# Kernel tuning notes

Hardware: AMD Instinct MI355X
Metric: run time of the kernel (lower is better)

Reference implementation:

```python
import jax, jax.numpy as jnp
import numpy as np

B, T, C, E = 8, 8192, 256, 64
CAPACITY_FACTOR = 1.25
TOP_K = 2


def setup_inputs() -> dict:
    key = jax.random.key(0)
    k1, k2, k3 = jax.random.split(key, 3)
    x = jax.random.normal(k1, (B, T, C), dtype=jnp.float32)
    W_gate = jax.random.normal(k2, (C, E), dtype=jnp.float32) / np.sqrt(C)
    W_experts = jax.random.normal(k3, (E, C, C), dtype=jnp.float32) / np.sqrt(C)
    return {"x": x, "W_gate": W_gate, "W_experts": W_experts}


def reference(x, W_gate, W_experts):
    b, t, c = x.shape
    e = W_gate.shape[1]
    n = b * t              # tokens
    s = n * TOP_K          # assignment slots, ordered (token i, slot j) like the torch loop
    capacity = max(1, int(CAPACITY_FACTOR * s / e))  # static python int

    logits = x @ W_gate                              # [B,T,E]
    gates = jax.nn.softmax(logits, axis=-1)
    scores, indices = jax.lax.top_k(gates, TOP_K)    # [B,T,2] (values are raw gate probs, no renorm)

    x_flat = x.reshape(n, c)
    eid = indices.reshape(s)                         # expert id per assignment, FIFO order i*2+j
    sc = scores.reshape(s)
    tok = jnp.repeat(jnp.arange(n), TOP_K)           # source token per assignment

    # FIFO rank of each assignment within its expert (matches the python capacity loop)
    onehot = jax.nn.one_hot(eid, e, dtype=jnp.int32)          # [S,E]
    rank = jnp.cumsum(onehot, axis=0)[jnp.arange(s), eid] - 1  # prior count of same expert
    keep = rank < capacity                                     # capacity-dropped tokens

    # Scatter tokens into per-expert buffers [E*capacity, C]; dropped slots go OOB -> 'drop'
    buf_idx = jnp.where(keep, eid * capacity + rank, e * capacity)
    buf = jnp.zeros((e * capacity, c), x.dtype).at[buf_idx].set(x_flat[tok], mode="drop")

    # Grouped GEMM: one Linear(C,C) per expert
    y = jnp.einsum("eck,ekd->ecd", buf.reshape(e, capacity, c), W_experts)
    y = y.reshape(e * capacity, c)

    # Gather back, scale by gate score, scatter-add into token positions
    safe_idx = jnp.where(keep, buf_idx, 0)
    contrib = jnp.where(keep[:, None], y[safe_idx] * sc[:, None], jnp.zeros((), x.dtype))
    combined = jnp.zeros((n, c), x.dtype).at[tok].add(contrib).reshape(b, t, c)

    load = gates.mean(axis=(0, 1))                  # [E]
    aux_loss = jnp.mean((load - 1.0 / e) ** 2)      # mse vs uniform
    return combined, aux_loss
```

## Files before the change

### kernel.cpp

```cpp
#include <hip/hip_runtime.h>
#include <stdint.h>

#define N_TOK   65536
#define S_SLOTS 131072
#define NEXP    64
#define CDIM    256
#define CAP     2560
#define NCHUNK  1024

typedef unsigned short u16;
typedef float    fvec4  __attribute__((ext_vector_type(4)));
typedef float    f32x4  __attribute__((ext_vector_type(4)));
typedef __bf16   bf16x8 __attribute__((ext_vector_type(8)));
typedef unsigned short u16x4 __attribute__((ext_vector_type(4)));

typedef __attribute__((address_space(1))) const void gvoid_t;
typedef __attribute__((address_space(3))) void       svoid_t;

__device__ __forceinline__ u16 f2bf(float f) {
  uint32_t u = __builtin_bit_cast(uint32_t, f);
  u += 0x7fffu + ((u >> 16) & 1u);
  return (u16)(u >> 16);
}
__device__ __forceinline__ float bf2f(u16 h) {
  return __builtin_bit_cast(float, (uint32_t)h << 16);
}
__device__ __forceinline__ void gload16(const void* g, void* l) {
  __builtin_amdgcn_global_load_lds(
      reinterpret_cast<gvoid_t*>(reinterpret_cast<uintptr_t>(g)),
      reinterpret_cast<svoid_t*>(reinterpret_cast<uintptr_t>(l)),
      16, 0, 0);
}

__global__ __launch_bounds__(256) void gating_kernel(
    const float* __restrict__ x, const float* __restrict__ Wg,
    u16* __restrict__ x_bf16, float* __restrict__ slot_score,
    int* __restrict__ slot_eid, float* __restrict__ load_g,
    int* __restrict__ chunk_hist)
{
  __shared__ float smem[8448];
  __shared__ int   hist_s[64];
  float* W_s   = smem;
  float* A_s   = smem + 4096;
  float* L_s   = smem;
  float* PMAXs = smem + 4160;
  float* PV1   = smem + 4416;
  int*   PI1   = (int*)(smem + 4672);
  float* PV2   = smem + 4928;
  int*   PI2   = (int*)(smem + 5184);
  float* PSUM  = smem + 5440;
  float* RINVs = smem + 5696;
  float* PLOAD = smem + 5760;

  const int t  = threadIdx.x;
  const int m0 = blockIdx.x * 64;
  const int ty = t >> 4, tx = t & 15;

  if (t < 64) hist_s[t] = 0;

  float acc[4][4];
#pragma unroll
  for (int j = 0; j < 4; ++j)
#pragma unroll
    for (int i = 0; i < 4; ++i) acc[j][i] = 0.f;

  for (int kt = 0; kt < 4; ++kt) {
    const int k0 = kt * 64;
#pragma unroll
    for (int p = 0; p < 4; ++p) {
      int idx = p * 1024 + t * 4;
      int kk = idx >> 6, e = idx & 63;
      *(fvec4*)&W_s[kk * 64 + e] = *(const fvec4*)&Wg[(size_t)(k0 + kk) * 64 + e];
    }
#pragma unroll
    for (int p = 0; p < 4; ++p) {
      int idx = p * 1024 + t * 4;
      int m = idx >> 6, k = idx & 63;
      fvec4 v = *(const fvec4*)&x[(size_t)(m0 + m) * 256 + k0 + k];
      *(fvec4*)&A_s[m * 68 + k] = v;
      u16x4 h;
      h.x = f2bf(v.x); h.y = f2bf(v.y); h.z = f2bf(v.z); h.w = f2bf(v.w);
      *(u16x4*)&x_bf16[(size_t)(m0 + m) * 256 + k0 + k] = h;
    }
    __syncthreads();
#pragma unroll
    for (int k4 = 0; k4 < 16; ++k4) {
      fvec4 av[4], bv[4];
#pragma unroll
      for (int j = 0; j < 4; ++j)
        av[j] = *(const fvec4*)&A_s[(ty * 4 + j) * 68 + k4 * 4];
#pragma unroll
      for (int kk = 0; kk < 4; ++kk)
        bv[kk] = *(const fvec4*)&W_s[(k4 * 4 + kk) * 64 + tx * 4];
#pragma unroll
      for (int j = 0; j < 4; ++j)
#pragma unroll
        for (int i = 0; i < 4; ++i) {
          acc[j][i] = fmaf(av[j][0], bv[0][i], acc[j][i]);
          acc[j][i] = fmaf(av[j][1], bv[1][i], acc[j][i]);
          acc[j][i] = fmaf(av[j][2], bv[2][i], acc[j][i]);
          acc[j][i] = fmaf(av[j][3], bv[3][i], acc[j][i]);
        }
    }
    __syncthreads();
  }

#pragma unroll
  for (int j = 0; j < 4; ++j)
#pragma unroll
    for (int i = 0; i < 4; ++i)
      L_s[(ty * 4 + j) * 65 + tx * 4 + i] = acc[j][i];
  __syncthreads();

  const int w = t >> 6, lane = t & 63;

  float pm = -3.4e38f, a1 = -3.4e38f, a2 = -3.4e38f;
  int   j1 = 0, j2 = 0;
#pragma unroll
  for (int ii = 0; ii < 16; ++ii) {
    int e = w * 16 + ii;
    float lg = L_s[lane * 65 + e];
    pm = fmaxf(pm, lg);
    if (lg > a1)      { a2 = a1; j2 = j1; a1 = lg; j1 = e; }
    else if (lg > a2) { a2 = lg; j2 = e; }
  }
  PMAXs[w * 64 + lane] = pm;
  PV1[w * 64 + lane] = a1; PI1[w * 64 + lane] = j1;
  PV2[w * 64 + lane] = a2; PI2[w * 64 + lane] = j2;
  __syncthreads();

  float m  = PMAXs[lane];
  float v1 = PV1[lane]; int i1 = PI1[lane];
  float v2 = PV2[lane]; int i2 = PI2[lane];
#pragma unroll
  for (int ww = 1; ww < 4; ++ww) {
    m = fmaxf(m, PMAXs[ww * 64 + lane]);
    float b1 = PV1[ww * 64 + lane]; int bi1 = PI1[ww * 64 + lane];
    float b2 = PV2[ww * 64 + lane]; int bi2 = PI2[ww * 64 + lane];
    if (b1 > v1) {
      if (v1 >= b2) { v2 = v1; i2 = i1; } else { v2 = b2; i2 = bi2; }
      v1 = b1; i1 = bi1;
    } else if (b1 > v2) { v2 = b1; i2 = bi1; }
  }

  float s = 0.f;
#pragma unroll
  for (int ii = 0; ii < 16; ++ii) {
    int e = w * 16 + ii;
    float E = __expf(L_s[lane * 65 + e] - m);
    L_s[lane * 65 + e] = E;
    s += E;
  }
  PSUM[w * 64 + lane] = s;
  __syncthreads();

  if (w == 0) {
    float rs = PSUM[lane] + PSUM[64 + lane] + PSUM[128 + lane] + PSUM[192 + lane];
    float ri = 1.0f / rs;
    RINVs[lane] = ri;
    float sc1 = L_s[lane * 65 + i1] * ri;
    float sc2 = L_s[lane * 65 + i2] * ri;
    int tg = m0 + lane;
    slot_eid[2 * tg]     = i1;
    slot_eid[2 * tg + 1] = i2;
    slot_score[2 * tg]     = sc1;
    slot_score[2 * tg + 1] = sc2;
    atomicAdd(&hist_s[i1], 1);
    atomicAdd(&hist_s[i2], 1);
  }
  __syncthreads();

  {
    float sl = 0.f;
#pragma unroll
    for (int jj = 0; jj < 16; ++jj) {
      int j = w * 16 + jj;
      sl = fmaf(L_s[j * 65 + lane], RINVs[j], sl);
    }
    PLOAD[t] = sl;
  }
  __syncthreads();
  if (t < 64) {
    float sl = PLOAD[t] + PLOAD[64 + t] + PLOAD[128 + t] + PLOAD[192 + t];
    atomicAdd(&load_g[t], sl);
    chunk_hist[blockIdx.x * 64 + t] = hist_s[t];
  }
}

__global__ __launch_bounds__(256) void wtrans_kernel(
    const float* __restrict__ W, u16* __restrict__ WT)
{
  __shared__ float tile[64 * 65];
  const int b = blockIdx.x;
  const int e = b >> 4, tt = b & 15;
  const int k0 = (tt >> 2) * 64, d0 = (tt & 3) * 64;
  const int t = threadIdx.x;
  const int j = t & 63, i0 = t >> 6;
  const float* We = W + (size_t)e * 65536;
#pragma unroll
  for (int p = 0; p < 16; ++p) {
    int i = p * 4 + i0;
    tile[i * 65 + j] = We[(size_t)(k0 + i) * 256 + d0 + j];
  }
  __syncthreads();
  u16* WTe = WT + (size_t)e * 65536;
#pragma unroll
  for (int p = 0; p < 16; ++p) {
    int d = p * 4 + i0;
    WTe[(size_t)(d0 + d) * 256 + k0 + j] = f2bf(tile[j * 65 + d]);
  }
}

__global__ __launch_bounds__(256) void scan_kernel(int* __restrict__ hist)
{
  const int e = blockIdx.x;
  const int t = threadIdx.x;
  const int lane = t & 63, w = t >> 6;
  int h[4];
#pragma unroll
  for (int i = 0; i < 4; ++i) h[i] = hist[(t * 4 + i) * 64 + e];
  int local = h[0] + h[1] + h[2] + h[3];
  int v = local;
#pragma unroll
  for (int off = 1; off < 64; off <<= 1) {
    int u = __shfl_up(v, off);
    if (lane >= off) v += u;
  }
  __shared__ int wtot[4];
  if (lane == 63) wtot[w] = v;
  __syncthreads();
  int woff = 0;
  for (int i = 0; i < w; ++i) woff += wtot[i];
  int excl = woff + v - local;
  hist[(t * 4 + 0) * 64 + e] = excl;
  hist[(t * 4 + 1) * 64 + e] = excl + h[0];
  hist[(t * 4 + 2) * 64 + e] = excl + h[0] + h[1];
  hist[(t * 4 + 3) * 64 + e] = excl + h[0] + h[1] + h[2];
}

__global__ __launch_bounds__(128) void rank_kernel(
    const int* __restrict__ slot_eid, const int* __restrict__ base,
    int* __restrict__ slot2buf, int* __restrict__ row_token)
{
  const int c = blockIdx.x;
  const int t = threadIdx.x;
  const int s = c * 128 + t;
  const int lane = t & 63, w = t >> 6;
  const int e = slot_eid[s];
  __shared__ int hist0[64];
  if (t < 64) hist0[t] = 0;
  __syncthreads();
  int rank = 0, cnt = 0;
#pragma unroll
  for (int k = 0; k < 64; ++k) {
    int eo = __shfl(e, k);
    bool m = (eo == e);
    rank += (m && k < lane) ? 1 : 0;
    cnt  += m ? 1 : 0;
  }
  if (w == 0 && rank == cnt - 1) hist0[e] = cnt;
  __syncthreads();
  int g = base[c * 64 + e] + rank + (w ? hist0[e] : 0);
  if (g < CAP) {
    slot2buf[s] = e * CAP + g;
    row_token[e * CAP + g] = s >> 1;
  } else {
    slot2buf[s] = -1;
  }
}

__global__ __launch_bounds__(256) void gemm_kernel(
    const u16* __restrict__ x_bf16, const u16* __restrict__ WT,
    const int* __restrict__ row_token, u16* __restrict__ y)
{
  __shared__ u16 A_s[128 * 32];
  __shared__ u16 B_s[128 * 32];
  __shared__ int tok_s[128];

  const int b = blockIdx.x;
  const int e = b / 40;
  const int r = b % 40;
  const int m0 = (r >> 1) * 128, n0 = (r & 1) * 128;
  const int t = threadIdx.x;

  if (t < 128) tok_s[t] = row_token[e * CAP + m0 + t];
  __syncthreads();

  const int w = t >> 6, lane = t & 63;
  const int rsub = lane >> 2;
  const int koff = (lane & 3) * 8;

  const int ra0 = w * 32 + rsub;
  const int ra1 = ra0 + 16;
  const char* pa0 = (const char*)(x_bf16 + (size_t)tok_s[ra0] * 256 + koff);
  const char* pa1 = (const char*)(x_bf16 + (size_t)tok_s[ra1] * 256 + koff);
  const u16* WTe = WT + (size_t)e * 65536;
  const char* pb0 = (const char*)(WTe + (size_t)(n0 + ra0) * 256 + koff);
  const char* pb1 = (const char*)(WTe + (size_t)(n0 + ra1) * 256 + koff);

  char* ldsA0 = (char*)A_s + (w * 32) * 64;
  char* ldsA1 = (char*)A_s + (w * 32 + 16) * 64;
  char* ldsB0 = (char*)B_s + (w * 32) * 64;
  char* ldsB1 = (char*)B_s + (w * 32 + 16) * 64;

  const int wm = w & 1, wn = w >> 1;
  const int lr = lane & 15, q = lane >> 4;

  f32x4 acc[4][4];
#pragma unroll
  for (int mt = 0; mt < 4; ++mt)
#pragma unroll
    for (int nt = 0; nt < 4; ++nt) acc[mt][nt] = (f32x4){0.f, 0.f, 0.f, 0.f};

  for (int kt = 0; kt < 8; ++kt) {
    gload16(pa0, ldsA0);
    gload16(pa1, ldsA1);
    gload16(pb0, ldsB0);
    gload16(pb1, ldsB1);
    __syncthreads();
    bf16x8 af[4], bg[4];
#pragma unroll
    for (int mt = 0; mt < 4; ++mt)
      af[mt] = *(const bf16x8*)&A_s[(wm * 64 + mt * 16 + lr) * 32 + q * 8];
#pragma unroll
    for (int nt = 0; nt < 4; ++nt)
      bg[nt] = *(const bf16x8*)&B_s[(wn * 64 + nt * 16 + lr) * 32 + q * 8];
#pragma unroll
    for (int mt = 0; mt < 4; ++mt)
#pragma unroll
      for (int nt = 0; nt < 4; ++nt)
        acc[mt][nt] = __builtin_amdgcn_mfma_f32_16x16x32_bf16(
            af[mt], bg[nt], acc[mt][nt], 0, 0, 0);
    __syncthreads();
    pa0 += 64; pa1 += 64; pb0 += 64; pb1 += 64;
  }

  u16* ye = y + (size_t)e * CAP * 256;
#pragma unroll
  for (int mt = 0; mt < 4; ++mt) {
    int grow = m0 + wm * 64 + mt * 16 + q * 4;
#pragma unroll
    for (int nt = 0; nt < 4; ++nt) {
      int gcol = n0 + wn * 64 + nt * 16 + lr;
#pragma unroll
      for (int rr = 0; rr < 4; ++rr)
        ye[(size_t)(grow + rr) * 256 + gcol] = f2bf(acc[mt][nt][rr]);
    }
  }
}

__global__ __launch_bounds__(256) void combine_kernel(
    const u16* __restrict__ y, const int* __restrict__ slot2buf,
    const float* __restrict__ slot_score, float* __restrict__ out)
{
  const int tok  = blockIdx.x * 4 + (threadIdx.x >> 6);
  const int lane = threadIdx.x & 63;
  const int   p0 = slot2buf[2 * tok],   p1 = slot2buf[2 * tok + 1];
  const float s0 = slot_score[2 * tok], s1 = slot_score[2 * tok + 1];
  float o0 = 0.f, o1 = 0.f, o2 = 0.f, o3 = 0.f;
  if (p0 >= 0) {
    u16x4 h = *(const u16x4*)&y[(size_t)p0 * 256 + lane * 4];
    o0 = fmaf(s0, bf2f(h.x), o0); o1 = fmaf(s0, bf2f(h.y), o1);
    o2 = fmaf(s0, bf2f(h.z), o2); o3 = fmaf(s0, bf2f(h.w), o3);
  }
  if (p1 >= 0) {
    u16x4 h = *(const u16x4*)&y[(size_t)p1 * 256 + lane * 4];
    o0 = fmaf(s1, bf2f(h.x), o0); o1 = fmaf(s1, bf2f(h.y), o1);
    o2 = fmaf(s1, bf2f(h.z), o2); o3 = fmaf(s1, bf2f(h.w), o3);
  }
  fvec4 o = {o0, o1, o2, o3};
  *(fvec4*)&out[(size_t)tok * 256 + lane * 4] = o;
}

__global__ __launch_bounds__(64) void aux_kernel(
    const float* __restrict__ load_g, float* __restrict__ out_aux)
{
  const int lane = threadIdx.x;
  float l = load_g[lane] * (1.0f / 65536.0f) - (1.0f / 64.0f);
  float v = l * l;
#pragma unroll
  for (int off = 1; off < 64; off <<= 1) v += __shfl_xor(v, off);
  if (lane == 0) out_aux[0] = v * (1.0f / 64.0f);
}

extern "C" void kernel_launch(void* const* d_in, const int* in_sizes, int n_in,
                              void* d_out, int out_size, void* d_ws, size_t ws_size,
                              hipStream_t stream)
{
  const float* x  = (const float*)d_in[0];
  const float* Wg = (const float*)d_in[1];
  const float* We = (const float*)d_in[2];
  float* out = (float*)d_out;

  char* ws = (char*)d_ws;
  float* slot_score = (float*)(ws + 0);
  int*   slot_eid   = (int*)(ws + 524288);
  int*   slot2buf   = (int*)(ws + 1048576);
  int*   row_token  = (int*)(ws + 1572864);
  float* load_g     = (float*)(ws + 2228224);
  int*   chunk_hist = (int*)(ws + 2359296);
  u16*   x_bf16     = (u16*)(ws + 4194304);
  u16*   WT         = (u16*)(ws + 37748736);
  u16*   y          = (u16*)(ws + 46137344);

  hipMemsetAsync(row_token, 0, 655360, stream);
  hipMemsetAsync(load_g, 0, 256, stream);

  gating_kernel<<<1024, 256, 0, stream>>>(x, Wg, x_bf16, slot_score, slot_eid,
                                          load_g, chunk_hist);
  wtrans_kernel<<<1024, 256, 0, stream>>>(We, WT);
  scan_kernel<<<64, 256, 0, stream>>>(chunk_hist);
  rank_kernel<<<1024, 128, 0, stream>>>(slot_eid, chunk_hist, slot2buf, row_token);
  gemm_kernel<<<2560, 256, 0, stream>>>(x_bf16, WT, row_token, y);
  combine_kernel<<<16384, 256, 0, stream>>>(y, slot2buf, slot_score, out);
  aux_kernel<<<1, 64, 0, stream>>>(load_g, out + 16777216);
}
```

Baseline: 239.0 us.

## Compute gating logits with split-bf16 MFMA instead of fp32 FMA

Replaces the fp32 scalar-FMA gating GEMM with bf16 MFMA instructions. Each fp32 operand is split into three bf16 parts (hi/mid/lo) and six cross products are accumulated to keep near-fp32 accuracy. A new small kernel pre-splits and transposes W_gate, and x tiles are loaded into LDS with direct global-to-LDS loads. The aim is to cut the compute cost of the gating matmul, at the price of an extra launch, the on-the-fly splitting work, and a small risk of top-k ties resolving differently.

Measured after the change: 242.2 us. Within noise of the previous version (+1.3%).

```diff
diff --git a/kernel.cpp b/kernel.cpp
--- a/kernel.cpp
+++ b/kernel.cpp
@@ -13,6 +13,7 @@
 typedef float    f32x4  __attribute__((ext_vector_type(4)));
 typedef __bf16   bf16x8 __attribute__((ext_vector_type(8)));
 typedef unsigned short u16x4 __attribute__((ext_vector_type(4)));
+typedef unsigned short u16x8 __attribute__((ext_vector_type(8)));
 
 typedef __attribute__((address_space(1))) const void gvoid_t;
 typedef __attribute__((address_space(3))) void       svoid_t;
@@ -32,87 +33,128 @@
       16, 0, 0);
 }
 
+__global__ __launch_bounds__(256) void wgsplit_kernel(
+    const float* __restrict__ Wg, u16* __restrict__ WgT_h,
+    u16* __restrict__ WgT_m, u16* __restrict__ WgT_l)
+{
+  __shared__ float tile[64 * 65];
+  const int k0 = blockIdx.x * 64;
+  const int t = threadIdx.x;
+  const int j = t & 63, i0 = t >> 6;
+#pragma unroll
+  for (int p = 0; p < 16; ++p) {
+    int i = p * 4 + i0;
+    tile[i * 65 + j] = Wg[(size_t)(k0 + i) * 64 + j];
+  }
+  __syncthreads();
+  const int e = t >> 2, kb = (t & 3) * 16;
+#pragma unroll
+  for (int p = 0; p < 16; ++p) {
+    int kk = kb + p;
+    float v = tile[kk * 65 + e];
+    u16 h  = f2bf(v); float r1 = v  - bf2f(h);
+    u16 md = f2bf(r1); float r2 = r1 - bf2f(md);
+    u16 l  = f2bf(r2);
+    size_t off = (size_t)e * 256 + k0 + kk;
+    WgT_h[off] = h; WgT_m[off] = md; WgT_l[off] = l;
+  }
+}
+
 __global__ __launch_bounds__(256) void gating_kernel(
-    const float* __restrict__ x, const float* __restrict__ Wg,
+    const float* __restrict__ x,
+    const u16* __restrict__ WgT_h, const u16* __restrict__ WgT_m,
+    const u16* __restrict__ WgT_l,
     u16* __restrict__ x_bf16, float* __restrict__ slot_score,
     int* __restrict__ slot_eid, float* __restrict__ load_g,
     int* __restrict__ chunk_hist)
 {
-  __shared__ float smem[8448];
-  __shared__ int   hist_s[64];
-  float* W_s   = smem;
-  float* A_s   = smem + 4096;
-  float* L_s   = smem;
-  float* PMAXs = smem + 4160;
-  float* PV1   = smem + 4416;
-  int*   PI1   = (int*)(smem + 4672);
-  float* PV2   = smem + 4928;
-  int*   PI2   = (int*)(smem + 5184);
-  float* PSUM  = smem + 5440;
-  float* RINVs = smem + 5696;
-  float* PLOAD = smem + 5760;
+  __shared__ char smem[32768];
+  __shared__ int  hist_s[64];
+  float* X_s = (float*)smem;
+  u16* A_h = (u16*)(smem + 8192);
+  u16* A_m = (u16*)(smem + 12288);
+  u16* A_l = (u16*)(smem + 16384);
+  u16* B_h = (u16*)(smem + 20480);
+  u16* B_m = (u16*)(smem + 24576);
+  u16* B_l = (u16*)(smem + 28672);
+  float* tf   = (float*)smem;
+  float* L_s  = tf;
+  float* PMAX = tf + 4160;
+  float* PV1  = tf + 4416;
+  int*   PI1  = (int*)(tf + 4672);
+  float* PV2  = tf + 4928;
+  int*   PI2  = (int*)(tf + 5184);
+  float* PSUM = tf + 5440;
+  float* RINV = tf + 5696;
+  float* PLOAD= tf + 5760;
 
   const int t  = threadIdx.x;
   const int m0 = blockIdx.x * 64;
-  const int ty = t >> 4, tx = t & 15;
+  const int w = t >> 6, lane = t & 63;
+  const int lr = lane & 15, q = lane >> 4;
+  const int srow = t >> 2;
+  const int scol = (t & 3) * 8;
 
   if (t < 64) hist_s[t] = 0;
 
-  float acc[4][4];
-#pragma unroll
-  for (int j = 0; j < 4; ++j)
-#pragma unroll
-    for (int i = 0; i < 4; ++i) acc[j][i] = 0.f;
-
-  for (int kt = 0; kt < 4; ++kt) {
-    const int k0 = kt * 64;
-#pragma unroll
-    for (int p = 0; p < 4; ++p) {
-      int idx = p * 1024 + t * 4;
-      int kk = idx >> 6, e = idx & 63;
-      *(fvec4*)&W_s[kk * 64 + e] = *(const fvec4*)&Wg[(size_t)(k0 + kk) * 64 + e];
+  f32x4 acc[4];
+#pragma unroll
+  for (int nt = 0; nt < 4; ++nt) acc[nt] = (f32x4){0.f, 0.f, 0.f, 0.f};
+
+  const float* gx = x + (size_t)(m0 + w * 16 + (lane >> 3)) * 256 + (lane & 7) * 4;
+  const size_t wgoff = (size_t)(w * 16 + (lane >> 2)) * 256 + (lane & 3) * 8;
+
+  for (int kt = 0; kt < 8; ++kt) {
+    __syncthreads();
+    gload16(gx + kt * 32,            (char*)X_s + w * 2048);
+    gload16(gx + kt * 32 + 8 * 256,  (char*)X_s + w * 2048 + 1024);
+    gload16(WgT_h + wgoff + kt * 32, (char*)B_h + w * 1024);
+    gload16(WgT_m + wgoff + kt * 32, (char*)B_m + w * 1024);
+    gload16(WgT_l + wgoff + kt * 32, (char*)B_l + w * 1024);
+    __syncthreads();
+
+    {
+      float v[8];
+      *(fvec4*)&v[0] = *(const fvec4*)&X_s[srow * 32 + scol];
+      *(fvec4*)&v[4] = *(const fvec4*)&X_s[srow * 32 + scol + 4];
+      u16x8 hv, mv, lv;
+#pragma unroll
+      for (int i = 0; i < 8; ++i) {
+        float f = v[i];
+        u16 h  = f2bf(f); float r1 = f  - bf2f(h);
+        u16 md = f2bf(r1); float r2 = r1 - bf2f(md);
+        hv[i] = h; mv[i] = md; lv[i] = f2bf(r2);
+      }
+      *(u16x8*)&A_h[srow * 32 + scol] = hv;
+      *(u16x8*)&A_m[srow * 32 + scol] = mv;
+      *(u16x8*)&A_l[srow * 32 + scol] = lv;
+      *(u16x8*)&x_bf16[(size_t)(m0 + srow) * 256 + kt * 32 + scol] = hv;
     }
-#pragma unroll
-    for (int p = 0; p < 4; ++p) {
-      int idx = p * 1024 + t * 4;
-      int m = idx >> 6, k = idx & 63;
-      fvec4 v = *(const fvec4*)&x[(size_t)(m0 + m) * 256 + k0 + k];
-      *(fvec4*)&A_s[m * 68 + k] = v;
-      u16x4 h;
-      h.x = f2bf(v.x); h.y = f2bf(v.y); h.z = f2bf(v.z); h.w = f2bf(v.w);
-      *(u16x4*)&x_bf16[(size_t)(m0 + m) * 256 + k0 + k] = h;
+
+    bf16x8 ah = *(const bf16x8*)&A_h[(w * 16 + lr) * 32 + q * 8];
+    bf16x8 am = *(const bf16x8*)&A_m[(w * 16 + lr) * 32 + q * 8];
+    bf16x8 al = *(const bf16x8*)&A_l[(w * 16 + lr) * 32 + q * 8];
+#pragma unroll
+    for (int nt = 0; nt < 4; ++nt) {
+      bf16x8 bh = *(const bf16x8*)&B_h[(nt * 16 + lr) * 32 + q * 8];
+      bf16x8 bm = *(const bf16x8*)&B_m[(nt * 16 + lr) * 32 + q * 8];
+      bf16x8 bl = *(const bf16x8*)&B_l[(nt * 16 + lr) * 32 + q * 8];
+      acc[nt] = __builtin_amdgcn_mfma_f32_16x16x32_bf16(ah, bh, acc[nt], 0, 0, 0);
+      acc[nt] = __builtin_amdgcn_mfma_f32_16x16x32_bf16(ah, bm, acc[nt], 0, 0, 0);
+      acc[nt] = __builtin_amdgcn_mfma_f32_16x16x32_bf16(am, bh, acc[nt], 0, 0, 0);
+      acc[nt] = __builtin_amdgcn_mfma_f32_16x16x32_bf16(am, bm, acc[nt], 0, 0, 0);
+      acc[nt] = __builtin_amdgcn_mfma_f32_16x16x32_bf16(ah, bl, acc[nt], 0, 0, 0);
+      acc[nt] = __builtin_amdgcn_mfma_f32_16x16x32_bf16(al, bh, acc[nt], 0, 0, 0);
     }
-    __syncthreads();
-#pragma unroll
-    for (int k4 = 0; k4 < 16; ++k4) {
-      fvec4 av[4], bv[4];
-#pragma unroll
-      for (int j = 0; j < 4; ++j)
-        av[j] = *(const fvec4*)&A_s[(ty * 4 + j) * 68 + k4 * 4];
-#pragma unroll
-      for (int kk = 0; kk < 4; ++kk)
-        bv[kk] = *(const fvec4*)&W_s[(k4 * 4 + kk) * 64 + tx * 4];
-#pragma unroll
-      for (int j = 0; j < 4; ++j)
-#pragma unroll
-        for (int i = 0; i < 4; ++i) {
-          acc[j][i] = fmaf(av[j][0], bv[0][i], acc[j][i]);
-          acc[j][i] = fmaf(av[j][1], bv[1][i], acc[j][i]);
-          acc[j][i] = fmaf(av[j][2], bv[2][i], acc[j][i]);
-          acc[j][i] = fmaf(av[j][3], bv[3][i], acc[j][i]);
-        }
-    }
-    __syncthreads();
-  }
-
-#pragma unroll
-  for (int j = 0; j < 4; ++j)
-#pragma unroll
-    for (int i = 0; i < 4; ++i)
-      L_s[(ty * 4 + j) * 65 + tx * 4 + i] = acc[j][i];
-  __syncthreads();
-
-  const int w = t >> 6, lane = t & 63;
+  }
+  __syncthreads();
+
+#pragma unroll
+  for (int nt = 0; nt < 4; ++nt)
+#pragma unroll
+    for (int rr = 0; rr < 4; ++rr)
+      L_s[(w * 16 + q * 4 + rr) * 65 + nt * 16 + lr] = acc[nt][rr];
+  __syncthreads();
 
   float pm = -3.4e38f, a1 = -3.4e38f, a2 = -3.4e38f;
   int   j1 = 0, j2 = 0;
@@ -124,17 +166,17 @@
     if (lg > a1)      { a2 = a1; j2 = j1; a1 = lg; j1 = e; }
     else if (lg > a2) { a2 = lg; j2 = e; }
   }
-  PMAXs[w * 64 + lane] = pm;
+  PMAX[w * 64 + lane] = pm;
   PV1[w * 64 + lane] = a1; PI1[w * 64 + lane] = j1;
   PV2[w * 64 + lane] = a2; PI2[w * 64 + lane] = j2;
   __syncthreads();
 
-  float m  = PMAXs[lane];
+  float mx = PMAX[lane];
   float v1 = PV1[lane]; int i1 = PI1[lane];
   float v2 = PV2[lane]; int i2 = PI2[lane];
 #pragma unroll
   for (int ww = 1; ww < 4; ++ww) {
-    m = fmaxf(m, PMAXs[ww * 64 + lane]);
+    mx = fmaxf(mx, PMAX[ww * 64 + lane]);
     float b1 = PV1[ww * 64 + lane]; int bi1 = PI1[ww * 64 + lane];
     float b2 = PV2[ww * 64 + lane]; int bi2 = PI2[ww * 64 + lane];
     if (b1 > v1) {
@@ -147,7 +189,7 @@
 #pragma unroll
   for (int ii = 0; ii < 16; ++ii) {
     int e = w * 16 + ii;
-    float E = __expf(L_s[lane * 65 + e] - m);
+    float E = __expf(L_s[lane * 65 + e] - mx);
     L_s[lane * 65 + e] = E;
     s += E;
   }
@@ -157,7 +199,7 @@
   if (w == 0) {
     float rs = PSUM[lane] + PSUM[64 + lane] + PSUM[128 + lane] + PSUM[192 + lane];
     float ri = 1.0f / rs;
-    RINVs[lane] = ri;
+    RINV[lane] = ri;
     float sc1 = L_s[lane * 65 + i1] * ri;
     float sc2 = L_s[lane * 65 + i2] * ri;
     int tg = m0 + lane;
@@ -175,7 +217,7 @@
 #pragma unroll
     for (int jj = 0; jj < 16; ++jj) {
       int j = w * 16 + jj;
-      sl = fmaf(L_s[j * 65 + lane], RINVs[j], sl);
+      sl = fmaf(L_s[j * 65 + lane], RINV[j], sl);
     }
     PLOAD[t] = sl;
   }
@@ -399,6 +441,9 @@
   int*   row_token  = (int*)(ws + 1572864);
   float* load_g     = (float*)(ws + 2228224);
   int*   chunk_hist = (int*)(ws + 2359296);
+  u16*   WgT_h      = (u16*)(ws + 2621440);
+  u16*   WgT_m      = (u16*)(ws + 2654208);
+  u16*   WgT_l      = (u16*)(ws + 2686976);
   u16*   x_bf16     = (u16*)(ws + 4194304);
   u16*   WT         = (u16*)(ws + 37748736);
   u16*   y          = (u16*)(ws + 46137344);
@@ -406,8 +451,9 @@
   hipMemsetAsync(row_token, 0, 655360, stream);
   hipMemsetAsync(load_g, 0, 256, stream);
 
-  gating_kernel<<<1024, 256, 0, stream>>>(x, Wg, x_bf16, slot_score, slot_eid,
-                                          load_g, chunk_hist);
+  wgsplit_kernel<<<4, 256, 0, stream>>>(Wg, WgT_h, WgT_m, WgT_l);
+  gating_kernel<<<1024, 256, 0, stream>>>(x, WgT_h, WgT_m, WgT_l, x_bf16,
+                                          slot_score, slot_eid, load_g, chunk_hist);
   wtrans_kernel<<<1024, 256, 0, stream>>>(We, WT);
   scan_kernel<<<64, 256, 0, stream>>>(chunk_hist);
   rank_kernel<<<1024, 128, 0, stream>>>(slot_eid, chunk_hist, slot2buf, row_token);
```
